# Kernel tuning notes

Hardware: AMD Instinct MI355X
Metric: run time of the kernel (lower is better)

The kernel has to match this reference:

```python
import jax, jax.numpy as jnp
import numpy as np

B, T, E, H = 64, 26, 300, 1024
FEAT, C = 2048, 7
S = C * C                  # 49 spatial positions
MCBD = 5000                # MCB_output_dim
D1 = MCBD * S              # mcb1 sketch dim = 245000
D2 = MCBD                  # mcb2 sketch dim
MCB_OUT, FACTOR = 1000, 5
VOCAB = 3000
EPS = 1e-12


def _count_sketch(x, h, s, d):
    # x: (B, n), h: (n,) int32 in [0, d), s: (n,) +-1 float -> (B, d)
    return jnp.zeros((x.shape[0], d), x.dtype).at[:, h].add(x * s)


def _cbp(x, y, hx, sx, hy, sy, d):
    # Compact bilinear pooling: count sketch both inputs, convolve via FFT.
    fx = jnp.fft.rfft(_count_sketch(x, hx, sx, d), n=d, axis=-1)
    fy = jnp.fft.rfft(_count_sketch(y, hy, sy, d), n=d, axis=-1)
    return jnp.fft.irfft(fx * fy, n=d, axis=-1)


def _lstm(x, W_ih, W_hh, b_ih, b_hh):
    # x: (T, B, E) -> hs: (T, B, H); torch gate order i, f, g, o
    xW = jnp.einsum('tbe,ge->tbg', x, W_ih) + b_ih + b_hh
    h0 = jnp.zeros((x.shape[1], W_hh.shape[1]), x.dtype)
    def step(carry, xt):
        h, c = carry
        g = xt + h @ W_hh.T
        i, f, gg, o = jnp.split(g, 4, axis=-1)
        c = jax.nn.sigmoid(f) * c + jax.nn.sigmoid(i) * jnp.tanh(gg)
        h = jax.nn.sigmoid(o) * jnp.tanh(c)
        return (h, c), h
    _, hs = jax.lax.scan(step, (h0, h0), xW)
    return hs


def _signed_sqrt(x):
    # sqrt(relu(x)) - sqrt(relu(-x)) == sign(x) * sqrt(|x|)
    return jnp.sign(x) * jnp.sqrt(jnp.abs(x))


def _l2norm(x):
    # F.normalize(x, dim=1)
    return x / jnp.maximum(jnp.linalg.norm(x, axis=1, keepdims=True), EPS)


def setup_inputs():
    key = jax.random.key(0)
    ks = jax.random.split(key, 32)
    f = lambda k, shp, sc=1.0: jax.random.normal(k, shp, jnp.float32) * sc
    ri = lambda k, shp, mx: jax.random.randint(k, shp, 0, mx, jnp.int32)
    return {
        'ques_embed': f(ks[0], (B, T, E)),
        'img_feat': f(ks[1], (B, C, C, FEAT)),
        'W_ih': f(ks[2], (4 * H, E), 0.02),
        'W_hh': f(ks[3], (4 * H, H), 0.02),
        'b_ih': f(ks[4], (4 * H,), 0.02),
        'b_hh': f(ks[5], (4 * H,), 0.02),
        'Wq1': f(ks[6], (512, H), 0.02),
        'bq1': f(ks[7], (512,), 0.02),
        'Wq2': f(ks[8], (2, 512), 0.02),
        'bq2': f(ks[9], (2,), 0.02),
        'Wi1': f(ks[10], (512, MCB_OUT), 0.02),
        'bi1': f(ks[11], (512,), 0.02),
        'Wi2': f(ks[12], (2, 512), 0.02),
        'bi2': f(ks[13], (2,), 0.02),
        'Wp': f(ks[14], (VOCAB, MCB_OUT), 0.02),
        'bp': f(ks[15], (VOCAB,), 0.02),
        'h1x': ri(ks[16], (FEAT * S,), D1),
        's1x': ri(ks[17], (FEAT * S,), 2),
        'h1q': ri(ks[18], (2 * H,), D1),
        's1q': ri(ks[19], (2 * H,), 2),
        'h2i': ri(ks[20], (2 * FEAT,), D2),
        's2i': ri(ks[21], (2 * FEAT,), 2),
        'h2q': ri(ks[22], (2 * H,), D2),
        's2q': ri(ks[23], (2 * H,), 2),
    }


def reference(ques_embed, img_feat, W_ih, W_hh, b_ih, b_hh, Wq1, bq1, Wq2, bq2,
              Wi1, bi1, Wi2, bi2, Wp, bp,
              h1x, s1x, h1q, s1q, h2i, s2i, h2q, s2q):
    sgn = lambda s: (2 * s - 1).astype(jnp.float32)
    img = jnp.transpose(img_feat, (0, 3, 1, 2)).reshape(B, FEAT, S)  # (B, feat, S)
    hs = _lstm(jnp.transpose(ques_embed, (1, 0, 2)), W_ih, W_hh, b_ih, b_hh)
    lstm1 = jnp.transpose(hs, (1, 2, 0))  # (B, H, T)
    # --- question attention (1x1 convs over (H, T)) ---
    qa = jax.nn.relu(jnp.einsum('oh,bht->bot', Wq1, lstm1) + bq1[None, :, None])
    qa = jnp.einsum('go,bot->bgt', Wq2, qa) + bq2[None, :, None]
    qatt = jax.nn.softmax(qa, axis=-1)  # (B, 2, T)
    q_feat = jnp.einsum('bgt,bht->bgh', qatt, lstm1).reshape(B, 2 * H)  # (B, 2048)
    # --- image attention with MCB1 ---
    iq = _cbp(img.reshape(B, FEAT * S), q_feat, h1x, sgn(s1x), h1q, sgn(s1q), D1)
    # (B, 5000*S) -> view (B,5000,S) -> split 5000 into (1000,5), sum factor -> (B,1000,S)
    iq = iq.reshape(B, MCB_OUT, FACTOR, S).sum(axis=2)
    iq = _l2norm(_signed_sqrt(iq).reshape(B, MCB_OUT * S)).reshape(B, MCB_OUT, S)
    ia = jax.nn.relu(jnp.einsum('om,bms->bos', Wi1, iq) + bi1[None, :, None])
    ia = jnp.einsum('go,bos->bgs', Wi2, ia) + bi2[None, :, None]
    iatt = jax.nn.softmax(ia, axis=-1)  # (B, 2, S)
    i_feat = jnp.einsum('bgs,bfs->bgf', iatt, img).reshape(B, 2 * FEAT)  # (B, 4096)
    # --- fine-grained fusion MCB2 ---
    z = _cbp(i_feat, q_feat, h2i, sgn(s2i), h2q, sgn(s2q), D2)
    z = z.reshape(B, MCB_OUT, FACTOR).sum(axis=2)
    z = _l2norm(_signed_sqrt(z))
    return jax.nn.softmax(z @ Wp.T + bp, axis=1)
```

## Files before the change

kernel.cpp:

```cpp
#include <hip/hip_runtime.h>
#include <hip/hip_fp16.h>
#include <math.h>

static constexpr int BB = 64, TT = 26, EE = 300, HH = 1024;
static constexpr int FEAT = 2048, SS = 49;
static constexpr int D1 = 245000, D2 = 5000;
static constexpr int MOUT = 1000;
static constexpr int VOCAB = 3000;

static constexpr int UPAD = 1008;
static constexpr int FOLD_R = 16000;
static constexpr int FOLD_NR = 16;
static constexpr int BCAP = 8192;
static constexpr int NITEMS = FEAT * SS;

template <int BM, int BN, int BK, int TM, int TN, bool RELU>
__global__ void gemm_abt(const float* __restrict__ A, const float* __restrict__ B,
                         const float* __restrict__ bias1, const float* __restrict__ bias2,
                         float* __restrict__ C,
                         int M, int N, int K, int lda, int ldb, int ldc) {
    constexpr int THREADS = (BM / TM) * (BN / TN);
    __shared__ __align__(16) float As[BK][BM + 4];
    __shared__ __align__(16) float Bs[BK][BN + 4];
    const int tid = threadIdx.x;
    const int tx = tid % (BN / TN);
    const int ty = tid / (BN / TN);
    const int block_m = blockIdx.y * BM;
    const int block_n = blockIdx.x * BN;
    float acc[TM][TN];
#pragma unroll
    for (int i = 0; i < TM; i++)
#pragma unroll
        for (int j = 0; j < TN; j++) acc[i][j] = 0.f;

    for (int k0 = 0; k0 < K; k0 += BK) {
        for (int i = tid; i < BM * BK; i += THREADS) {
            int m = i / BK, kk = i % BK;
            int gm = block_m + m, gk = k0 + kk;
            As[kk][m] = (gm < M && gk < K) ? A[(size_t)gm * lda + gk] : 0.f;
        }
        for (int i = tid; i < BN * BK; i += THREADS) {
            int n = i / BK, kk = i % BK;
            int gn = block_n + n, gk = k0 + kk;
            Bs[kk][n] = (gn < N && gk < K) ? B[(size_t)gn * ldb + gk] : 0.f;
        }
        __syncthreads();
#pragma unroll
        for (int kk = 0; kk < BK; kk++) {
            float a[TM], b[TN];
            if constexpr ((TM & 3) == 0 && (TN & 3) == 0) {
#pragma unroll
                for (int i = 0; i < TM / 4; i++) {
                    float4 t4 = *reinterpret_cast<const float4*>(&As[kk][ty * TM + 4 * i]);
                    a[4 * i] = t4.x; a[4 * i + 1] = t4.y;
                    a[4 * i + 2] = t4.z; a[4 * i + 3] = t4.w;
                }
#pragma unroll
                for (int j = 0; j < TN / 4; j++) {
                    float4 t4 = *reinterpret_cast<const float4*>(&Bs[kk][tx * TN + 4 * j]);
                    b[4 * j] = t4.x; b[4 * j + 1] = t4.y;
                    b[4 * j + 2] = t4.z; b[4 * j + 3] = t4.w;
                }
            } else {
#pragma unroll
                for (int i = 0; i < TM; i++) a[i] = As[kk][ty * TM + i];
#pragma unroll
                for (int j = 0; j < TN; j++) b[j] = Bs[kk][tx * TN + j];
            }
#pragma unroll
            for (int i = 0; i < TM; i++)
#pragma unroll
                for (int j = 0; j < TN; j++) acc[i][j] += a[i] * b[j];
        }
        __syncthreads();
    }
#pragma unroll
    for (int i = 0; i < TM; i++) {
        int gm = block_m + ty * TM + i;
        if (gm >= M) continue;
#pragma unroll
        for (int j = 0; j < TN; j++) {
            int gn = block_n + tx * TN + j;
            if (gn >= N) continue;
            float v = acc[i][j];
            if (bias1) v += bias1[gn];
            if (bias2) v += bias2[gn];
            if (RELU) v = fmaxf(v, 0.f);
            C[(size_t)gm * ldc + gn] = v;
        }
    }
}

__global__ void xwt_transpose(const float* __restrict__ xw, float* __restrict__ xwT) {
    __shared__ float L[64][65];
    const int t = blockIdx.x;
    const int g0 = blockIdx.y * 64;
    const int tid = threadIdx.x;
    for (int u = 0; u < 16; u++) {
        int idx = u * 256 + tid;
        int b = idx >> 6, g = idx & 63;
        L[g][b] = xw[((size_t)b * TT + t) * 4096 + g0 + g];
    }
    __syncthreads();
    for (int u = 0; u < 16; u++) {
        int idx = u * 256 + tid;
        int g = idx >> 6, b = idx & 63;
        xwT[((size_t)t * 4096 + g0 + g) * 64 + b] = L[g][b];
    }
}

__global__ void __launch_bounds__(256, 2)
lstm_step4(const float* __restrict__ xwT, const float* __restrict__ W_hh,
           const float* __restrict__ hin, float* __restrict__ hout,
           float* __restrict__ cst, float* __restrict__ hs, int step) {
    __shared__ __align__(16) float hch[2][128][64];
    __shared__ __align__(16) float wch[2][16][128];
    const int tid = threadIdx.x;
    const int hh0 = blockIdx.x * 4;
    float* part = (float*)wch;

    if (step > 0) {
        const int lr = tid >> 4;
        const int b4 = tid & 15;
        float acc0 = 0.f, acc1 = 0.f, acc2 = 0.f, acc3 = 0.f;
        {
            const float4* hsrc = (const float4*)hin;
            float4* hdst = (float4*)hch[0];
#pragma unroll
            for (int u = 0; u < 8; u++) hdst[tid + 256 * u] = hsrc[tid + 256 * u];
#pragma unroll
            for (int u = 0; u < 2; u++) {
                int f4 = tid + 256 * u;
                int lr4 = f4 >> 5, c = f4 & 31;
                const float4* wsrc = (const float4*)(
                    W_hh + ((size_t)((lr4 >> 2) * 1024 + hh0 + (lr4 & 3))) * 1024);
                ((float4*)wch[0])[f4] = wsrc[c];
            }
        }
        __syncthreads();
        for (int ck = 0; ck < 8; ck++) {
            const int cur = ck & 1;
            float4 hreg[8];
            float4 wreg[2];
            if (ck < 7) {
                const float4* hsrc = (const float4*)(hin + (ck + 1) * 8192);
#pragma unroll
                for (int u = 0; u < 8; u++) hreg[u] = hsrc[tid + 256 * u];
#pragma unroll
                for (int u = 0; u < 2; u++) {
                    int f4 = tid + 256 * u;
                    int lr4 = f4 >> 5, c = f4 & 31;
                    const float4* wsrc = (const float4*)(
                        W_hh + ((size_t)((lr4 >> 2) * 1024 + hh0 + (lr4 & 3))) * 1024 +
                        (ck + 1) * 128);
                    wreg[u] = wsrc[c];
                }
            }
#pragma unroll 8
            for (int k4 = 0; k4 < 32; k4++) {
                float4 wv = *(const float4*)&wch[cur][lr][k4 * 4];
#pragma unroll
                for (int e = 0; e < 4; e++) {
                    float w = (&wv.x)[e];
                    float4 hv = *(const float4*)&hch[cur][k4 * 4 + e][b4 * 4];
                    acc0 = fmaf(w, hv.x, acc0);
                    acc1 = fmaf(w, hv.y, acc1);
                    acc2 = fmaf(w, hv.z, acc2);
                    acc3 = fmaf(w, hv.w, acc3);
                }
            }
            if (ck < 7) {
                float4* hdst = (float4*)hch[cur ^ 1];
#pragma unroll
                for (int u = 0; u < 8; u++) hdst[tid + 256 * u] = hreg[u];
#pragma unroll
                for (int u = 0; u < 2; u++) ((float4*)wch[cur ^ 1])[tid + 256 * u] = wreg[u];
            }
            __syncthreads();
        }
        part[(lr * 64) + b4 * 4 + 0] = acc0;
        part[(lr * 64) + b4 * 4 + 1] = acc1;
        part[(lr * 64) + b4 * 4 + 2] = acc2;
        part[(lr * 64) + b4 * 4 + 3] = acc3;
        __syncthreads();
    }
    {
        const int i = tid >> 6;
        const int b = tid & 63;
        const int row = hh0 + i;
        const int idx = row * 64 + b;
        float g4[4];
#pragma unroll
        for (int j = 0; j < 4; j++) {
            float sum = xwT[((size_t)step * 4096 + j * 1024 + row) * 64 + b];
            if (step > 0) sum += part[(j * 4 + i) * 64 + b];
            g4[j] = sum;
        }
        float si = 1.f / (1.f + expf(-g4[0]));
        float sf = 1.f / (1.f + expf(-g4[1]));
        float tg = tanhf(g4[2]);
        float so = 1.f / (1.f + expf(-g4[3]));
        float cp = (step > 0) ? cst[idx] : 0.f;
        float cn = sf * cp + si * tg;
        cst[idx] = cn;
        float hn = so * tanhf(cn);
        hout[idx] = hn;
        hs[((size_t)step * BB + b) * HH + row] = hn;
    }
}

__global__ void qa2_wave(const float* __restrict__ qa, const float* __restrict__ Wq2,
                         const float* __restrict__ bq2, float* __restrict__ out) {
    int wv = (blockIdx.x * blockDim.x + threadIdx.x) >> 6;
    int lane = threadIdx.x & 63;
    if (wv >= BB * 2 * TT) return;
    int t = wv % TT;
    int bg = wv / TT;
    int g = bg & 1;
    const float* arow = qa + ((size_t)t * BB + (bg >> 1)) * 512;
    const float* wrow = Wq2 + g * 512;
    float acc = 0.f;
#pragma unroll
    for (int o = 0; o < 8; o++) acc += wrow[lane + 64 * o] * arow[lane + 64 * o];
    for (int off = 32; off; off >>= 1) acc += __shfl_down(acc, off);
    if (lane == 0) out[wv] = acc + bq2[g];
}

__global__ void ia2_wave(const float* __restrict__ ia, const float* __restrict__ Wi2,
                         const float* __restrict__ bi2, float* __restrict__ out) {
    int wv = (blockIdx.x * blockDim.x + threadIdx.x) >> 6;
    int lane = threadIdx.x & 63;
    if (wv >= BB * 2 * SS) return;
    int s = wv % SS;
    int bg = wv / SS;
    int g = bg & 1;
    const float* arow = ia + ((size_t)(bg >> 1) * SS + s) * 512;
    const float* wrow = Wi2 + g * 512;
    float acc = 0.f;
#pragma unroll
    for (int o = 0; o < 8; o++) acc += wrow[lane + 64 * o] * arow[lane + 64 * o];
    for (int off = 32; off; off >>= 1) acc += __shfl_down(acc, off);
    if (lane == 0) out[wv] = acc + bi2[g];
}

__global__ void softmax_wave(float* __restrict__ x, int rows, int len) {
    int wv = (blockIdx.x * blockDim.x + threadIdx.x) >> 6;
    int lane = threadIdx.x & 63;
    if (wv >= rows) return;
    float* xr = x + (size_t)wv * len;
    float v = (lane < len) ? xr[lane] : -1e30f;
    float m = v;
    for (int off = 32; off; off >>= 1) m = fmaxf(m, __shfl_xor(m, off));
    float e = (lane < len) ? expf(v - m) : 0.f;
    float ssum = e;
    for (int off = 32; off; off >>= 1) ssum += __shfl_xor(ssum, off);
    if (lane < len) xr[lane] = e / ssum;
}

__global__ void qfeat_kernel(const float* __restrict__ qatt, const float* __restrict__ hs,
                             float* __restrict__ qf) {
    int idx = blockIdx.x * blockDim.x + threadIdx.x;
    if (idx >= BB * 2048) return;
    int b = idx >> 11;
    int gh = idx & 2047;
    int g = gh >> 10;
    int hh = gh & 1023;
    float acc = 0.f;
    for (int t = 0; t < TT; t++)
        acc += qatt[((size_t)b * 2 + g) * TT + t] * hs[((size_t)t * BB + b) * HH + hh];
    qf[idx] = acc;
}

__global__ void bucket_build(const int* __restrict__ h1x, const int* __restrict__ s1x,
                             int* __restrict__ bcnt, int* __restrict__ bkh,
                             int* __restrict__ bkp) {
    __shared__ int lcnt[FOLD_NR], lbase[FOLD_NR];
    const int tid = threadIdx.x;
    if (tid < FOLD_NR) lcnt[tid] = 0;
    __syncthreads();
    const int i = blockIdx.x * 256 + tid;
    int h = 0, pay = 0, r1 = -1, r2 = -1, p1 = 0, p2 = 0;
    if (i < NITEMS) {
        h = h1x[i];
        int f = i / SS, s = i - f * SS;
        pay = (s * FEAT + f) | (s1x[i] << 31);
#pragma unroll
        for (int r = 0; r < FOLD_NR; r++) {
            int dd = h - r * FOLD_R;
            if (dd < 0) dd += D1;
            if (dd < FOLD_R + 196) {
                int p = atomicAdd(&lcnt[r], 1);
                if (r1 < 0) { r1 = r; p1 = p; }
                else        { r2 = r; p2 = p; }
            }
        }
    }
    __syncthreads();
    if (tid < FOLD_NR) lbase[tid] = atomicAdd(&bcnt[tid], lcnt[tid]);
    __syncthreads();
    if (r1 >= 0) {
        int pos = lbase[r1] + p1;
        if (pos < BCAP) { bkh[r1 * BCAP + pos] = h; bkp[r1 * BCAP + pos] = pay; }
    }
    if (r2 >= 0) {
        int pos = lbase[r2] + p2;
        if (pos < BCAP) { bkh[r2 * BCAP + pos] = h; bkp[r2 * BCAP + pos] = pay; }
    }
}

__global__ void sketch_fold2(const float* __restrict__ img_feat, const int* __restrict__ bcnt,
                             const int* __restrict__ bkh, const int* __restrict__ bkp,
                             float* __restrict__ afold) {
    __shared__ float sl[FOLD_R + 196];
    const int r = blockIdx.x;
    const int b = blockIdx.y;
    const int r0 = r * FOLD_R;
    for (int i = threadIdx.x; i < FOLD_R + 196; i += 256) sl[i] = 0.f;
    __syncthreads();
    const int n = min(bcnt[r], BCAP);
    const float* __restrict__ ib = img_feat + (size_t)b * NITEMS;
    for (int j = threadIdx.x; j < n; j += 256) {
        int h = bkh[r * BCAP + j];
        int pay = bkp[r * BCAP + j];
        int d = h - r0;
        if (d < 0) d += D1;
        float v = ib[pay & 0x7FFFFFFF];
        float val = ((unsigned)pay >> 31) ? v : -v;
        atomicAdd(&sl[d], val);
    }
    __syncthreads();
    float* ab = afold + (size_t)b * D1;
    for (int t = threadIdx.x; t < FOLD_R; t += 256) {
        int g = r0 + t;
        if (g >= D1) break;
        ab[g] = sl[t] + sl[t + 49] + sl[t + 98] + sl[t + 147] + sl[t + 196];
    }
}

__global__ void transpose_f16b(const float* __restrict__ afold, __half2* __restrict__ A2) {
    __shared__ float L[64][65];
    const int t0 = blockIdx.x * 64;
    const int tid = threadIdx.x;
    for (int c = 0; c < 16; c++) {
        int idx = c * 256 + tid;
        int b = idx >> 6, i = idx & 63;
        int t = t0 + i;
        L[i][b] = (t < D1) ? afold[(size_t)b * D1 + t] : 0.f;
    }
    __syncthreads();
    for (int c = 0; c < 8; c++) {
        int u8 = c * 256 + tid;
        int t_loc = u8 >> 5, qq = u8 & 31;
        int t = t0 + t_loc;
        if (t >= D1) continue;
        __half2 v = __halves2half2(__float2half_rn(L[t_loc][2 * qq]),
                                   __float2half_rn(L[t_loc][2 * qq + 1]));
        int u = t / 245;
        int dv = t - u * 245;
        A2[((size_t)dv * UPAD + u) * 32 + qq] = v;
        if (u < 8) A2[((size_t)dv * UPAD + 1000 + u) * 32 + qq] = v;
    }
}

__global__ void sort_tab(const int* __restrict__ h1q, int2* __restrict__ tab2) {
    __shared__ int k[2048], v[2048];
    const int s = blockIdx.x;
    const int t = threadIdx.x;
#pragma unroll
    for (int e = 0; e < 2; e++) {
        int j = t + e * 1024;
        int d = s - h1q[j];
        if (d < 0) d += D1;
        int du = d / 245;
        int dv = d - du * 245;
        k[j] = ((dv * UPAD + du) << 10) | du;
        v[j] = j;
    }
    for (int size = 2; size <= 2048; size <<= 1) {
        for (int stride = size >> 1; stride > 0; stride >>= 1) {
            __syncthreads();
            int pos = 2 * t - (t & (stride - 1));
            bool asc = ((pos & size) == 0);
            int a = k[pos], b2 = k[pos + stride];
            if ((a > b2) == asc) {
                k[pos] = b2; k[pos + stride] = a;
                int tmp = v[pos]; v[pos] = v[pos + stride]; v[pos + stride] = tmp;
            }
        }
    }
    __syncthreads();
#pragma unroll
    for (int e = 0; e < 2; e++) {
        int r = t + e * 1024;
        tab2[(size_t)s * 2048 + r] = make_int2(k[r], v[r]);
    }
}

__global__ void vts_build(const float* __restrict__ qf, const int* __restrict__ s1q,
                          __half2* __restrict__ vTs) {
    int gid = blockIdx.x * blockDim.x + threadIdx.x;
    if (gid >= 2048 * 32) return;
    int j = gid >> 5, q = gid & 31;
    float sg = (float)(2 * s1q[j] - 1);
    vTs[gid] = __halves2half2(__float2half_rn(qf[(size_t)(2 * q) * 2048 + j] * sg),
                              __float2half_rn(qf[(size_t)(2 * q + 1) * 2048 + j] * sg));
}

__global__ void vs_permute(const __half2* __restrict__ vTs, const int2* __restrict__ tab2,
                           __half2* __restrict__ vS) {
    int gid = blockIdx.x * 256 + threadIdx.x;
    if (gid >= SS * 2048 * 32) return;
    int q = gid & 31;
    int sr = gid >> 5;
    int j = tab2[sr].y;
    vS[gid] = vTs[j * 32 + q];
}

__global__ void __launch_bounds__(256, 8)
mcb1_gather8(const __half2* __restrict__ A2, const __half2* __restrict__ vS,
             const int2* __restrict__ tab2, float* __restrict__ iq) {
    __shared__ int sp[2176];
    const int wid = blockIdx.x;
    const int lin = (wid & 7) * 196 + (wid >> 3);
    const int s = lin >> 5;
    const int bx = lin & 31;
    const int tid = threadIdx.x;
    for (int i = tid; i < 2048; i += 256) sp[i] = tab2[(size_t)s * 2048 + i].x;
    __syncthreads();

    const int q = tid & 31;
    const int w = tid >> 5;
    const int mgrp = w & 3;
    const int jh = w >> 2;
    const int m0 = bx * 32 + mgrp * 8;
    const int m0c = (m0 <= 992) ? m0 : 992;
    const int m0w = m0c - 1000;
    const int thr = 1000 - m0c;

    float accL[8], accH[8];
#pragma unroll
    for (int kk = 0; kk < 8; kk++) { accL[kk] = 0.f; accH[kk] = 0.f; }

    const unsigned* __restrict__ vp =
        (const unsigned*)vS + (((size_t)s * 2048 + (jh << 10)) << 5) + q;
    const unsigned* __restrict__ abase = (const unsigned*)A2 + q;
    const int rbase = jh << 10;

#pragma unroll 2
    for (int r = 0; r < 1024; ++r) {
        int key = sp[rbase + r];
        int A = key >> 10;
        int du = key & 1023;
        int t = A + ((du >= thr) ? m0w : m0c);
        const unsigned* __restrict__ arow = abase + ((size_t)t << 5);
        unsigned vv = vp[(size_t)r << 5];
#pragma unroll
        for (int kk = 0; kk < 8; kk++) {
            unsigned a = arow[kk * 32];
            asm("v_fma_mix_f32 %0, %1, %2, %0 op_sel:[0,0,0] op_sel_hi:[1,1,0]"
                : "+v"(accL[kk]) : "v"(a), "v"(vv));
            asm("v_fma_mix_f32 %0, %1, %2, %0 op_sel:[1,1,0] op_sel_hi:[1,1,0]"
                : "+v"(accH[kk]) : "v"(a), "v"(vv));
        }
    }

    __syncthreads();
    float* red = (float*)sp;
    const int slot = mgrp * 32 + q;
    if (jh == 1) {
        float* dst = red + slot * 17;
#pragma unroll
        for (int kk = 0; kk < 8; kk++) { dst[kk] = accL[kk]; dst[kk + 8] = accH[kk]; }
    }
    __syncthreads();
    if (jh == 0 && m0 <= 992) {
        const float* srcp = red + slot * 17;
        float* o0 = iq + ((size_t)(2 * q) * SS + s) * MOUT + m0;
        float* o1 = o0 + (size_t)SS * MOUT;
#pragma unroll
        for (int kk = 0; kk < 8; kk++) {
            o0[kk] = accL[kk] + srcp[kk];
            o1[kk] = accH[kk] + srcp[kk + 8];
        }
    }
}

__global__ void ssqrt_l2norm(float* __restrict__ x, int n) {
    __shared__ float red[1024];
    __shared__ float inv_s;
    const int nt = blockDim.x;
    int b = blockIdx.x;
    float* xb = x + (size_t)b * n;
    float ss = 0.f;
    for (int i = threadIdx.x; i < n; i += nt) {
        float v = xb[i];
        float y = (v >= 0.f) ? sqrtf(v) : -sqrtf(-v);
        xb[i] = y;
        ss += y * y;
    }
    red[threadIdx.x] = ss;
    __syncthreads();
    for (int s = nt >> 1; s > 0; s >>= 1) {
        if (threadIdx.x < s) red[threadIdx.x] += red[threadIdx.x + s];
        __syncthreads();
    }
    if (threadIdx.x == 0) inv_s = 1.f / fmaxf(sqrtf(red[0]), 1e-12f);
    __syncthreads();
    float inv = inv_s;
    for (int i = threadIdx.x; i < n; i += nt) xb[i] *= inv;
}

__global__ void ifeat_kernel(const float* __restrict__ iatt, const float* __restrict__ img_feat,
                             float* __restrict__ ifeat) {
    int idx = blockIdx.x * blockDim.x + threadIdx.x;
    if (idx >= BB * 4096) return;
    int b = idx >> 12;
    int gf = idx & 4095;
    int g = gf >> 11;
    int f = gf & 2047;
    float acc = 0.f;
    for (int s = 0; s < SS; s++)
        acc += iatt[((size_t)b * 2 + g) * SS + s] * img_feat[((size_t)b * SS + s) * FEAT + f];
    ifeat[idx] = acc;
}

__global__ void mcb2_scatter(const float* __restrict__ ifeat, const int* __restrict__ h2i,
                             const int* __restrict__ s2i, float* __restrict__ atil2) {
    int tid = blockIdx.x * blockDim.x + threadIdx.x;
    if (tid >= BB * 4096) return;
    int i = tid & 4095;
    int b = tid >> 12;
    float v = ifeat[tid] * (float)(2 * s2i[i] - 1);
    int p = h2i[i];
    float* ab = atil2 + (size_t)b * D2;
#pragma unroll
    for (int f = 0; f < 5; f++) {
        int t = p - f;
        if (t < 0) t += D2;
        atomicAdd(&ab[t], v);
    }
}

__global__ void mcb2_gather(const float* __restrict__ atil2, const float* __restrict__ qf,
                            const int* __restrict__ h2q, const int* __restrict__ s2q,
                            float* __restrict__ z) {
    __shared__ float sa[D2];
    __shared__ int sp[2048];
    __shared__ float sv[2048];
    int b = blockIdx.y;
    for (int i = threadIdx.x; i < D2; i += 256) sa[i] = atil2[(size_t)b * D2 + i];
    const float* qb = qf + (size_t)b * 2048;
    for (int j = threadIdx.x; j < 2048; j += 256) {
        sp[j] = h2q[j];
        sv[j] = qb[j] * (float)(2 * s2q[j] - 1);
    }
    __syncthreads();
    int m = blockIdx.x * 256 + threadIdx.x;
    if (m >= MOUT) return;
    int base = 5 * m + D2;
    float acc = 0.f;
#pragma unroll 4
    for (int j = 0; j < 2048; j++) {
        int addr = base - sp[j];
        if (addr >= D2) addr -= D2;
        acc += sv[j] * sa[addr];
    }
    z[(size_t)b * MOUT + m] = acc;
}

__global__ void softmax_rows(const float* __restrict__ logits, float* __restrict__ out, int n) {
    __shared__ float red[1024];
    const int nt = blockDim.x;
    int b = blockIdx.x;
    const float* xr = logits + (size_t)b * n;
    float* orow = out + (size_t)b * n;
    float mx = -1e30f;
    for (int i = threadIdx.x; i < n; i += nt) mx = fmaxf(mx, xr[i]);
    red[threadIdx.x] = mx;
    __syncthreads();
    for (int s = nt >> 1; s > 0; s >>= 1) {
        if (threadIdx.x < s) red[threadIdx.x] = fmaxf(red[threadIdx.x], red[threadIdx.x + s]);
        __syncthreads();
    }
    mx = red[0];
    __syncthreads();
    float sum = 0.f;
    for (int i = threadIdx.x; i < n; i += nt) sum += expf(xr[i] - mx);
    red[threadIdx.x] = sum;
    __syncthreads();
    for (int s = nt >> 1; s > 0; s >>= 1) {
        if (threadIdx.x < s) red[threadIdx.x] += red[threadIdx.x + s];
        __syncthreads();
    }
    float inv = 1.f / red[0];
    for (int i = threadIdx.x; i < n; i += nt) orow[i] = expf(xr[i] - mx) * inv;
}

extern "C" void kernel_launch(void* const* d_in, const int* in_sizes, int n_in,
                              void* d_out, int out_size, void* d_ws, size_t ws_size,
                              hipStream_t stream) {
    (void)in_sizes; (void)n_in; (void)out_size; (void)ws_size;
    const float* ques = (const float*)d_in[0];
    const float* img  = (const float*)d_in[1];
    const float* W_ih = (const float*)d_in[2];
    const float* W_hh = (const float*)d_in[3];
    const float* b_ih = (const float*)d_in[4];
    const float* b_hh = (const float*)d_in[5];
    const float* Wq1  = (const float*)d_in[6];
    const float* bq1  = (const float*)d_in[7];
    const float* Wq2  = (const float*)d_in[8];
    const float* bq2  = (const float*)d_in[9];
    const float* Wi1  = (const float*)d_in[10];
    const float* bi1  = (const float*)d_in[11];
    const float* Wi2  = (const float*)d_in[12];
    const float* bi2  = (const float*)d_in[13];
    const float* Wp   = (const float*)d_in[14];
    const float* bpc  = (const float*)d_in[15];
    const int* h1x = (const int*)d_in[16];
    const int* s1x = (const int*)d_in[17];
    const int* h1q = (const int*)d_in[18];
    const int* s1q = (const int*)d_in[19];
    const int* h2i = (const int*)d_in[20];
    const int* s2i = (const int*)d_in[21];
    const int* h2q = (const int*)d_in[22];
    const int* s2q = (const int*)d_in[23];
    float* out = (float*)d_out;

    float* ws = (float*)d_ws;
    float* xw    = ws;
    float* hs    = ws + 6815744;
    float* hTa   = ws + 8519680;
    float* hTb   = ws + 8585216;
    float* cst   = ws + 8650752;
    float* qa    = ws + 10224640;
    float* qatt  = ws + 11076608;
    float* xwT   = ws + 11080704;
    float* afold = ws;
    float* iq     = ws;
    float* ia     = ws + 3136000;
    float* iatt   = ws + 4741632;
    float* ifeat  = ws + 4749824;
    float* atil2  = ws + 5011968;
    float* z      = ws + 5331968;
    float* logits = ws + 5395968;
    int2*  tab2   = (int2*)(ws + 5600000);
    __half2* vS   = (__half2*)(ws + 6000000);
    __half2* A2    = (__half2*)(ws + 15680000);
    float* qf      = ws + 15680000 + 7905536;
    __half2* vTs   = (__half2*)(qf + 131072);
    int* bcnt      = (int*)(ws + 15680000 + 7905536 + 131072 + 65536 + 4096);
    int* bkh       = bcnt + 64;
    int* bkp       = bkh + FOLD_NR * BCAP;

    (void)hipMemsetAsync(bcnt, 0, 64 * 4, stream);
    bucket_build<<<(NITEMS + 255) / 256, 256, 0, stream>>>(h1x, s1x, bcnt, bkh, bkp);

    {
        dim3 grid(4096 / 64, (BB * TT + 127) / 128);
        gemm_abt<128, 64, 16, 8, 4, false><<<grid, 256, 0, stream>>>(
            ques, W_ih, b_ih, b_hh, xw, BB * TT, 4 * HH, EE, EE, EE, 4 * HH);
    }
    {
        dim3 grid(TT, 64);
        xwt_transpose<<<grid, 256, 0, stream>>>(xw, xwT);
    }
    for (int t = 0; t < TT; t++) {
        float* hout = (t & 1) ? hTb : hTa;
        const float* hin = (t & 1) ? hTa : hTb;
        lstm_step4<<<256, 256, 0, stream>>>(xwT, W_hh, (t == 0) ? nullptr : hin,
                                            hout, cst, hs, t);
    }
    {
        dim3 grid(512 / 64, (TT * BB + 63) / 64);
        gemm_abt<64, 64, 16, 4, 4, true><<<grid, 256, 0, stream>>>(
            hs, Wq1, bq1, nullptr, qa, TT * BB, 512, HH, HH, HH, 512);
    }
    qa2_wave<<<(BB * 2 * TT * 64 + 255) / 256, 256, 0, stream>>>(qa, Wq2, bq2, qatt);
    softmax_wave<<<(BB * 2 * 64 + 255) / 256, 256, 0, stream>>>(qatt, BB * 2, TT);
    qfeat_kernel<<<(BB * 2048) / 256, 256, 0, stream>>>(qatt, hs, qf);
    {
        dim3 grid(FOLD_NR, BB);
        sketch_fold2<<<grid, 256, 0, stream>>>(img, bcnt, bkh, bkp, afold);
    }
    {
        int nblk = (D1 + 63) / 64;
        transpose_f16b<<<nblk, 256, 0, stream>>>(afold, A2);
    }
    sort_tab<<<SS, 1024, 0, stream>>>(h1q, tab2);
    vts_build<<<(2048 * 32) / 256, 256, 0, stream>>>(qf, s1q, vTs);
    vs_permute<<<(SS * 2048 * 32 + 255) / 256, 256, 0, stream>>>(vTs, tab2, vS);
    mcb1_gather8<<<1568, 256, 0, stream>>>(A2, vS, tab2, iq);
    ssqrt_l2norm<<<BB, 1024, 0, stream>>>(iq, MOUT * SS);
    {
        dim3 grid(512 / 64, (BB * SS + 63) / 64);
        gemm_abt<64, 64, 16, 4, 4, true><<<grid, 256, 0, stream>>>(
            iq, Wi1, bi1, nullptr, ia, BB * SS, 512, MOUT, MOUT, MOUT, 512);
    }
    ia2_wave<<<(BB * 2 * SS * 64 + 255) / 256, 256, 0, stream>>>(ia, Wi2, bi2, iatt);
    softmax_wave<<<(BB * 2 * 64 + 255) / 256, 256, 0, stream>>>(iatt, BB * 2, SS);
    ifeat_kernel<<<(BB * 4096) / 256, 256, 0, stream>>>(iatt, img, ifeat);
    (void)hipMemsetAsync(atil2, 0, (size_t)BB * D2 * 4, stream);
    mcb2_scatter<<<(BB * 4096) / 256, 256, 0, stream>>>(ifeat, h2i, s2i, atil2);
    {
        dim3 grid(4, BB);
        mcb2_gather<<<grid, 256, 0, stream>>>(atil2, qf, h2q, s2q, z);
    }
    ssqrt_l2norm<<<BB, 256, 0, stream>>>(z, MOUT);
    {
        dim3 grid((VOCAB + 63) / 64, 4);
        gemm_abt<16, 64, 16, 2, 2, false><<<grid, 256, 0, stream>>>(
            z, Wp, bpc, nullptr, logits, BB, VOCAB, MOUT, MOUT, MOUT, VOCAB);
    }
    softmax_rows<<<BB, 1024, 0, stream>>>(logits, out, VOCAB);
}
```

Before: 2.615 ms.

## Use fp16 MFMA GEMM kernel for the three large projection GEMMs

Adds a 64x64-tile GEMM that converts fp32 operands to fp16 on load into shared memory and computes with 16x16x32 f16 MFMA instructions with fp32 accumulation. It replaces the scalar fp32 tiled GEMM for the LSTM input projection, the question attention projection and the image attention projection. The goal is to move these GEMMs onto matrix cores, accepting reduced input precision. The kernel has no M/N bounds checks and assumes row counts are multiples of 64, which 1664 and 3136 satisfy. It also simplifies the old GEMM's shared-memory reads by dropping the float4 path.

```diff
diff --git a/kernel.cpp b/kernel.cpp
--- a/kernel.cpp
+++ b/kernel.cpp
@@ -13,6 +13,83 @@
 static constexpr int FOLD_NR = 16;
 static constexpr int BCAP = 8192;
 static constexpr int NITEMS = FEAT * SS;
+
+typedef __attribute__((ext_vector_type(8))) _Float16 f16x8;
+typedef __attribute__((ext_vector_type(4))) float f32x4;
+
+template <bool RELU>
+__global__ void __launch_bounds__(256, 8)
+gemm_mfma(const float* __restrict__ A, const float* __restrict__ B,
+          const float* __restrict__ bias1, const float* __restrict__ bias2,
+          float* __restrict__ C, int M, int N, int K,
+          int lda, int ldb, int ldc) {
+    __shared__ __align__(16) _Float16 As[64][40];
+    __shared__ __align__(16) _Float16 Bs[64][40];
+    const int tid = threadIdx.x;
+    const int bm = blockIdx.y * 64, bn = blockIdx.x * 64;
+    const int w = tid >> 6, lane = tid & 63;
+    const int wr = w >> 1, wc = w & 1;
+    const int fr = lane & 15, kg = lane >> 4;
+    f32x4 acc[2][2];
+#pragma unroll
+    for (int i = 0; i < 2; i++)
+#pragma unroll
+        for (int j = 0; j < 2; j++) acc[i][j] = (f32x4){0.f, 0.f, 0.f, 0.f};
+
+    const int r = tid >> 2;
+    const int kq = (tid & 3) * 8;
+
+    for (int k0 = 0; k0 < K; k0 += 32) {
+        {
+            _Float16 ta[8], tb[8];
+#pragma unroll
+            for (int e4 = 0; e4 < 2; e4++) {
+                int gk = k0 + kq + e4 * 4;
+                if (gk < K) {
+                    float4 va = *(const float4*)&A[(size_t)(bm + r) * lda + gk];
+                    float4 vb = *(const float4*)&B[(size_t)(bn + r) * ldb + gk];
+                    ta[e4*4+0] = (_Float16)va.x; ta[e4*4+1] = (_Float16)va.y;
+                    ta[e4*4+2] = (_Float16)va.z; ta[e4*4+3] = (_Float16)va.w;
+                    tb[e4*4+0] = (_Float16)vb.x; tb[e4*4+1] = (_Float16)vb.y;
+                    tb[e4*4+2] = (_Float16)vb.z; tb[e4*4+3] = (_Float16)vb.w;
+                } else {
+#pragma unroll
+                    for (int e = 0; e < 4; e++) { ta[e4*4+e] = (_Float16)0.f; tb[e4*4+e] = (_Float16)0.f; }
+                }
+            }
+            *(f16x8*)&As[r][kq] = *(f16x8*)ta;
+            *(f16x8*)&Bs[r][kq] = *(f16x8*)tb;
+        }
+        __syncthreads();
+        f16x8 af[2], bf[2];
+#pragma unroll
+        for (int i = 0; i < 2; i++) af[i] = *(const f16x8*)&As[wr * 32 + i * 16 + fr][kg * 8];
+#pragma unroll
+        for (int j = 0; j < 2; j++) bf[j] = *(const f16x8*)&Bs[wc * 32 + j * 16 + fr][kg * 8];
+#pragma unroll
+        for (int i = 0; i < 2; i++)
+#pragma unroll
+            for (int j = 0; j < 2; j++)
+                acc[i][j] = __builtin_amdgcn_mfma_f32_16x16x32_f16(af[i], bf[j], acc[i][j], 0, 0, 0);
+        __syncthreads();
+    }
+#pragma unroll
+    for (int i = 0; i < 2; i++)
+#pragma unroll
+        for (int j = 0; j < 2; j++) {
+            int col = bn + wc * 32 + j * 16 + fr;
+            float bv = 0.f;
+            if (bias1) bv += bias1[col];
+            if (bias2) bv += bias2[col];
+#pragma unroll
+            for (int rg = 0; rg < 4; rg++) {
+                int row = bm + wr * 32 + i * 16 + kg * 4 + rg;
+                float v = acc[i][j][rg] + bv;
+                if (RELU) v = fmaxf(v, 0.f);
+                C[(size_t)row * ldc + col] = v;
+            }
+        }
+}
 
 template <int BM, int BN, int BK, int TM, int TN, bool RELU>
 __global__ void gemm_abt(const float* __restrict__ A, const float* __restrict__ B,
@@ -48,25 +125,10 @@
 #pragma unroll
         for (int kk = 0; kk < BK; kk++) {
             float a[TM], b[TN];
-            if constexpr ((TM & 3) == 0 && (TN & 3) == 0) {
-#pragma unroll
-                for (int i = 0; i < TM / 4; i++) {
-                    float4 t4 = *reinterpret_cast<const float4*>(&As[kk][ty * TM + 4 * i]);
-                    a[4 * i] = t4.x; a[4 * i + 1] = t4.y;
-                    a[4 * i + 2] = t4.z; a[4 * i + 3] = t4.w;
-                }
-#pragma unroll
-                for (int j = 0; j < TN / 4; j++) {
-                    float4 t4 = *reinterpret_cast<const float4*>(&Bs[kk][tx * TN + 4 * j]);
-                    b[4 * j] = t4.x; b[4 * j + 1] = t4.y;
-                    b[4 * j + 2] = t4.z; b[4 * j + 3] = t4.w;
-                }
-            } else {
-#pragma unroll
-                for (int i = 0; i < TM; i++) a[i] = As[kk][ty * TM + i];
-#pragma unroll
-                for (int j = 0; j < TN; j++) b[j] = Bs[kk][tx * TN + j];
-            }
+#pragma unroll
+            for (int i = 0; i < TM; i++) a[i] = As[kk][ty * TM + i];
+#pragma unroll
+            for (int j = 0; j < TN; j++) b[j] = Bs[kk][tx * TN + j];
 #pragma unroll
             for (int i = 0; i < TM; i++)
 #pragma unroll
@@ -656,8 +718,8 @@
     bucket_build<<<(NITEMS + 255) / 256, 256, 0, stream>>>(h1x, s1x, bcnt, bkh, bkp);
 
     {
-        dim3 grid(4096 / 64, (BB * TT + 127) / 128);
-        gemm_abt<128, 64, 16, 8, 4, false><<<grid, 256, 0, stream>>>(
+        dim3 grid(4096 / 64, 1664 / 64);
+        gemm_mfma<false><<<grid, 256, 0, stream>>>(
             ques, W_ih, b_ih, b_hh, xw, BB * TT, 4 * HH, EE, EE, EE, 4 * HH);
     }
     {
@@ -671,8 +733,8 @@
                                             hout, cst, hs, t);
     }
     {
-        dim3 grid(512 / 64, (TT * BB + 63) / 64);
-        gemm_abt<64, 64, 16, 4, 4, true><<<grid, 256, 0, stream>>>(
+        dim3 grid(512 / 64, 1664 / 64);
+        gemm_mfma<true><<<grid, 256, 0, stream>>>(
             hs, Wq1, bq1, nullptr, qa, TT * BB, 512, HH, HH, HH, 512);
     }
     qa2_wave<<<(BB * 2 * TT * 64 + 255) / 256, 256, 0, stream>>>(qa, Wq2, bq2, qatt);
@@ -692,8 +754,8 @@
     mcb1_gather8<<<1568, 256, 0, stream>>>(A2, vS, tab2, iq);
     ssqrt_l2norm<<<BB, 1024, 0, stream>>>(iq, MOUT * SS);
     {
-        dim3 grid(512 / 64, (BB * SS + 63) / 64);
-        gemm_abt<64, 64, 16, 4, 4, true><<<grid, 256, 0, stream>>>(
+        dim3 grid(512 / 64, 3136 / 64);
+        gemm_mfma<true><<<grid, 256, 0, stream>>>(
             iq, Wi1, bi1, nullptr, ia, BB * SS, 512, MOUT, MOUT, MOUT, 512);
     }
     ia2_wave<<<(BB * 2 * SS * 64 + 255) / 256, 256, 0, stream>>>(ia, Wi2, bi2, iatt);
```

After: 2.212 ms. 1.18x faster.
